# Performance work log

Measured on AMD Instinct MI355X. Metric: run time of the kernel, lower is better.

The kernel has to match this reference:

```python
import jax, jax.numpy as jnp
import numpy as np

N_NODES = 100000
N_EDGES = 1600000
N_FEAT = 128
HIDDEN = 128
N_CLASSES = 10
N_GRAPHS = 512


def setup_inputs() -> dict:
    key = jax.random.key(0)
    ks = jax.random.split(key, 20)

    def lin(k, fan_in, fan_out, bias=True):
        kw, kb = jax.random.split(k)
        s = 1.0 / np.sqrt(fan_in)
        W = jax.random.uniform(kw, (fan_in, fan_out), jnp.float32, -s, s)
        if bias:
            b = jax.random.uniform(kb, (fan_out,), jnp.float32, -s, s)
            return W, b
        return W

    x = jax.random.normal(ks[0], (N_NODES, N_FEAT), jnp.float32)
    edge_index = jax.random.randint(ks[1], (2, N_EDGES), 0, N_NODES)
    batch = jnp.sort(jax.random.randint(ks[2], (N_NODES,), 0, N_GRAPHS))

    w1l, b1 = lin(ks[3], N_FEAT, HIDDEN)
    w1r = lin(ks[4], N_FEAT, HIDDEN, bias=False)
    w2l, b2 = lin(ks[5], HIDDEN, HIDDEN)
    w2r = lin(ks[6], HIDDEN, HIDDEN, bias=False)
    w3l, b3 = lin(ks[7], HIDDEN, HIDDEN)
    w3r = lin(ks[8], HIDDEN, HIDDEN, bias=False)
    gate_w, gate_b = lin(ks[9], HIDDEN, 1)
    lin1_w, lin1_b = lin(ks[10], HIDDEN, HIDDEN)
    lin2_w, lin2_b = lin(ks[11], HIDDEN, N_CLASSES)

    return dict(x=x, edge_index=edge_index, batch=batch,
                w1l=w1l, b1=b1, w1r=w1r,
                w2l=w2l, b2=b2, w2r=w2r,
                w3l=w3l, b3=b3, w3r=w3r,
                gate_w=gate_w, gate_b=gate_b,
                lin1_w=lin1_w, lin1_b=lin1_b,
                lin2_w=lin2_w, lin2_b=lin2_b)


def _sage_conv(x, src, dst, Wl, bl, Wr, n_nodes):
    # PyG SAGEConv(mean): out = lin_l(mean_{j in N(i)} x_j) + lin_r(x_i)
    msg_sum = jax.ops.segment_sum(x[src], dst, num_segments=n_nodes)
    cnt = jax.ops.segment_sum(jnp.ones((src.shape[0], 1), x.dtype), dst,
                              num_segments=n_nodes)
    mean = msg_sum / jnp.maximum(cnt, 1.0)
    return mean @ Wl + bl + x @ Wr


def reference(x, edge_index, batch,
              w1l, b1, w1r, w2l, b2, w2r, w3l, b3, w3r,
              gate_w, gate_b, lin1_w, lin1_b, lin2_w, lin2_b):
    n = x.shape[0]
    src, dst = edge_index[0], edge_index[1]

    h = jax.nn.relu(_sage_conv(x, src, dst, w1l, b1, w1r, n))
    h = jax.nn.relu(_sage_conv(h, src, dst, w2l, b2, w2r, n))
    h = jax.nn.relu(_sage_conv(h, src, dst, w3l, b3, w3r, n))

    # AttentionalAggregation: scatter-softmax of gate over graph segments
    gate = h @ gate_w + gate_b                                  # [N, 1]
    m = jax.ops.segment_max(gate, batch, num_segments=N_GRAPHS)  # [G, 1]
    e = jnp.exp(gate - m[batch])
    s = jax.ops.segment_sum(e, batch, num_segments=N_GRAPHS)     # [G, 1]
    alpha = e / s[batch]
    pooled = jax.ops.segment_sum(alpha * h, batch, num_segments=N_GRAPHS)  # [G, H]

    out = jax.nn.relu(pooled @ lin1_w + lin1_b)
    # dropout is identity in eval mode
    out = out @ lin2_w + lin2_b
    return jax.nn.log_softmax(out, axis=-1)
```

## Files before the change

### kernel.cpp

```cpp
#include <hip/hip_runtime.h>
#include <stdint.h>

#define N_NODES 100000
#define N_EDGES 1600000
#define NF 128
#define NG 512
#define NC 10

#define NBUCK ((N_NODES + 255) / 256)
#define EPB 4096

#define KSTRIDE 136
#define GEMM_B ((N_NODES + 127) / 128)

#define CVT_B 6250
#define BT_B 384
#define BOUNDS_B 3
#define COUNT_B ((N_EDGES + EPB - 1) / EPB)

typedef short short8 __attribute__((ext_vector_type(8)));
typedef float f32x4 __attribute__((ext_vector_type(4)));

__device__ __forceinline__ unsigned short f2b(float f) {
    unsigned u = __float_as_uint(f);
    u += 0x7fffu + ((u >> 16) & 1u);
    return (unsigned short)(u >> 16);
}
__device__ __forceinline__ unsigned cvt2(float lo, float hi) {
    unsigned r;
    asm("v_cvt_pk_bf16_f32 %0, %1, %2" : "=v"(r) : "v"(lo), "v"(hi));
    return r;
}
__device__ __forceinline__ float lo16(unsigned v) { return __uint_as_float(v << 16); }
__device__ __forceinline__ float hi16(unsigned v) { return __uint_as_float(v & 0xffff0000u); }

__global__ __launch_bounds__(256) void prep_kernel(const float* __restrict__ x, unsigned short* __restrict__ xb,
                                                   const float* __restrict__ w1l, const float* __restrict__ w1r,
                                                   const float* __restrict__ w2l, const float* __restrict__ w2r,
                                                   const float* __restrict__ w3l, const float* __restrict__ w3r,
                                                   unsigned short* __restrict__ Bt,
                                                   const int* __restrict__ batch, int* __restrict__ gstart,
                                                   const int* __restrict__ dst, int* __restrict__ bcount) {
    const int b = blockIdx.x, t = threadIdx.x;
    if (b < CVT_B) {
        int i = b * 256 + t;
        const float4* ip = (const float4*)x;
        float4 a = ip[2 * i], c = ip[2 * i + 1];
        uint4 o;
        o.x = cvt2(a.x, a.y);
        o.y = cvt2(a.z, a.w);
        o.z = cvt2(c.x, c.y);
        o.w = cvt2(c.z, c.w);
        ((uint4*)xb)[i] = o;
    } else if (b < CVT_B + BT_B) {
        int i = (b - CVT_B) * 256 + t;
        int layer = i / (128 * 256);
        int r = i % (128 * 256);
        int n = r / 256, k = r % 256;
        const float* wl = (layer == 0) ? w1l : (layer == 1) ? w2l : w3l;
        const float* wr = (layer == 0) ? w1r : (layer == 1) ? w2r : w3r;
        float v = (k < 128) ? wl[k * 128 + n] : wr[(k - 128) * 128 + n];
        Bt[i] = f2b(v);
    } else if (b < CVT_B + BT_B + BOUNDS_B) {
        int g = (b - CVT_B - BT_B) * 256 + t;
        if (g > NG) return;
        int lo = 0, hi = N_NODES;
        while (lo < hi) {
            int mid = (lo + hi) >> 1;
            if (batch[mid] < g) lo = mid + 1; else hi = mid;
        }
        gstart[g] = lo;
    } else {
        __shared__ int h[NBUCK];
        for (int i = t; i < NBUCK; i += 256) h[i] = 0;
        __syncthreads();
        const int base = (b - CVT_B - BT_B - BOUNDS_B) * EPB;
        const int lim = min(base + EPB, N_EDGES);
        for (int i = base + t; i < lim; i += 256) atomicAdd(&h[dst[i] >> 8], 1);
        __syncthreads();
        for (int i = t; i < NBUCK; i += 256)
            if (h[i]) atomicAdd(&bcount[i], h[i]);
    }
}

__global__ __launch_bounds__(512) void bucket_scan(const int* __restrict__ bcount, int* __restrict__ bbase,
                                                   int* __restrict__ gcursor, int* __restrict__ rowptr) {
    __shared__ int sh[512];
    const int t = threadIdx.x;
    int v = (t < NBUCK) ? bcount[t] : 0;
    sh[t] = v;
    __syncthreads();
    for (int off = 1; off < 512; off <<= 1) {
        int u = (t >= off) ? sh[t - off] : 0;
        __syncthreads();
        sh[t] += u;
        __syncthreads();
    }
    if (t < NBUCK) {
        int e = sh[t] - v;
        bbase[t] = e;
        gcursor[t] = e;
    }
    if (t == NBUCK - 1) bbase[NBUCK] = sh[t];
    if (t == 0) rowptr[N_NODES] = N_EDGES;
}

__global__ __launch_bounds__(256) void bucket_scatter(const int* __restrict__ src, const int* __restrict__ dst,
                                                      int* __restrict__ gcursor, unsigned* __restrict__ brec) {
    __shared__ int h[NBUCK];
    for (int i = threadIdx.x; i < NBUCK; i += 256) h[i] = 0;
    __syncthreads();
    const int base = blockIdx.x * EPB;
    const int lim = min(base + EPB, N_EDGES);
    for (int i = base + threadIdx.x; i < lim; i += 256) atomicAdd(&h[dst[i] >> 8], 1);
    __syncthreads();
    for (int i = threadIdx.x; i < NBUCK; i += 256) {
        int c = h[i];
        if (c) h[i] = atomicAdd(&gcursor[i], c);
    }
    __syncthreads();
    for (int i = base + threadIdx.x; i < lim; i += 256) {
        int d = dst[i];
        int pos = atomicAdd(&h[d >> 8], 1);
        brec[pos] = ((unsigned)(d & 255) << 17) | (unsigned)src[i];
    }
}

__global__ __launch_bounds__(256) void bucket_fill(const unsigned* __restrict__ brec, const int* __restrict__ bbase,
                                                   int* __restrict__ rowptr, int* __restrict__ eidx) {
    __shared__ int nh[256];
    __shared__ int sc[256];
    const int b = blockIdx.x, t = threadIdx.x;
    const int beg = bbase[b], end = bbase[b + 1];
    nh[t] = 0;
    __syncthreads();
    for (int i = beg + t; i < end; i += 256) atomicAdd(&nh[brec[i] >> 17], 1);
    __syncthreads();
    int cnt = nh[t];
    sc[t] = cnt;
    __syncthreads();
    for (int off = 1; off < 256; off <<= 1) {
        int u = (t >= off) ? sc[t - off] : 0;
        __syncthreads();
        sc[t] += u;
        __syncthreads();
    }
    int excl = sc[t] - cnt;
    int node = b * 256 + t;
    if (node < N_NODES) rowptr[node] = beg + excl;
    nh[t] = beg + excl;
    __syncthreads();
    for (int i = beg + t; i < end; i += 256) {
        unsigned r = brec[i];
        int pos = atomicAdd(&nh[r >> 17], 1);
        eidx[pos] = (int)(r & 0x1FFFFu);
    }
}

__global__ __launch_bounds__(256) void agg_kernel(const unsigned short* __restrict__ F,
                                                  const int* __restrict__ rowptr,
                                                  const int* __restrict__ eidx,
                                                  unsigned short* __restrict__ M) {
    int node = blockIdx.x * 4 + (threadIdx.x >> 6);
    if (node >= N_NODES) return;
    const int lane = threadIdx.x & 63;
    const int quad = lane >> 4, ql = lane & 15;
    const int beg = rowptr[node], end = rowptr[node + 1];
    const char* Fb = (const char*)F;
    const unsigned qoff = (unsigned)ql << 4;

    float a0 = 0.f, a1 = 0.f, a2 = 0.f, a3 = 0.f, a4 = 0.f, a5 = 0.f, a6 = 0.f, a7 = 0.f;

    for (int cs = beg; cs < end; cs += 64) {
        int e = cs + lane;
        int idx = eidx[e < end ? e : end - 1];
        int n = end - cs;
        if (n > 64) n = 64;
        const int nfull = n >> 4;
        int l = quad;
        for (int g = 0; g < nfull; ++g, l += 16) {
            int r0 = __shfl(idx, l);
            int r1 = __shfl(idx, l + 4);
            int r2 = __shfl(idx, l + 8);
            int r3 = __shfl(idx, l + 12);
            uint4 v0 = *(const uint4*)(Fb + (((unsigned)r0 << 8) | qoff));
            uint4 v1 = *(const uint4*)(Fb + (((unsigned)r1 << 8) | qoff));
            uint4 v2 = *(const uint4*)(Fb + (((unsigned)r2 << 8) | qoff));
            uint4 v3 = *(const uint4*)(Fb + (((unsigned)r3 << 8) | qoff));
            a0 += lo16(v0.x) + lo16(v1.x) + lo16(v2.x) + lo16(v3.x);
            a1 += hi16(v0.x) + hi16(v1.x) + hi16(v2.x) + hi16(v3.x);
            a2 += lo16(v0.y) + lo16(v1.y) + lo16(v2.y) + lo16(v3.y);
            a3 += hi16(v0.y) + hi16(v1.y) + hi16(v2.y) + hi16(v3.y);
            a4 += lo16(v0.z) + lo16(v1.z) + lo16(v2.z) + lo16(v3.z);
            a5 += hi16(v0.z) + hi16(v1.z) + hi16(v2.z) + hi16(v3.z);
            a6 += lo16(v0.w) + lo16(v1.w) + lo16(v2.w) + lo16(v3.w);
            a7 += hi16(v0.w) + hi16(v1.w) + hi16(v2.w) + hi16(v3.w);
        }
        const int base = nfull << 4;
        for (int it = base; it < n; it += 4) {
            int l0 = it + quad;
            int r0 = __shfl(idx, l0 < n ? l0 : n - 1);
            float s0 = (l0 < n) ? 1.f : 0.f;
            uint4 v0 = *(const uint4*)(Fb + (((unsigned)r0 << 8) | qoff));
            a0 += s0 * lo16(v0.x); a1 += s0 * hi16(v0.x);
            a2 += s0 * lo16(v0.y); a3 += s0 * hi16(v0.y);
            a4 += s0 * lo16(v0.z); a5 += s0 * hi16(v0.z);
            a6 += s0 * lo16(v0.w); a7 += s0 * hi16(v0.w);
        }
    }

    a0 += __shfl_xor(a0, 16); a0 += __shfl_xor(a0, 32);
    a1 += __shfl_xor(a1, 16); a1 += __shfl_xor(a1, 32);
    a2 += __shfl_xor(a2, 16); a2 += __shfl_xor(a2, 32);
    a3 += __shfl_xor(a3, 16); a3 += __shfl_xor(a3, 32);
    a4 += __shfl_xor(a4, 16); a4 += __shfl_xor(a4, 32);
    a5 += __shfl_xor(a5, 16); a5 += __shfl_xor(a5, 32);
    a6 += __shfl_xor(a6, 16); a6 += __shfl_xor(a6, 32);
    a7 += __shfl_xor(a7, 16); a7 += __shfl_xor(a7, 32);

    if (quad == 0) {
        float inv = 1.0f / (float)max(end - beg, 1);
        uint4 o;
        o.x = cvt2(a0 * inv, a1 * inv);
        o.y = cvt2(a2 * inv, a3 * inv);
        o.z = cvt2(a4 * inv, a5 * inv);
        o.w = cvt2(a6 * inv, a7 * inv);
        ((uint4*)M)[(size_t)node * 16 + ql] = o;
    }
}

__global__ __launch_bounds__(256, 4) void gemm_kernel(const unsigned short* __restrict__ Am,
                                                      const unsigned short* __restrict__ Ax,
                                                      const unsigned short* __restrict__ Bt,
                                                      const float* __restrict__ bias,
                                                      unsigned short* __restrict__ Out,
                                                      const float* __restrict__ gatew,
                                                      const float* __restrict__ gateb,
                                                      float* __restrict__ gate) {
    const int t = threadIdx.x;
    const int wave = t >> 6, lane = t & 63;
    const int lrow = lane & 15, quad = lane >> 4;
    const int row0 = blockIdx.x * 128 + wave * 32;

    __shared__ __attribute__((aligned(16))) unsigned short Bs[128 * KSTRIDE];

    f32x4 acc[2][8];
#pragma unroll
    for (int i = 0; i < 2; ++i)
#pragma unroll
        for (int j = 0; j < 8; ++j) acc[i][j] = (f32x4){0.f, 0.f, 0.f, 0.f};

    int arow0 = row0 + lrow;          if (arow0 > N_NODES - 1) arow0 = N_NODES - 1;
    int arow1 = row0 + 16 + lrow;     if (arow1 > N_NODES - 1) arow1 = N_NODES - 1;

    for (int p = 0; p < 2; ++p) {
        if (p) __syncthreads();
#pragma unroll
        for (int i = 0; i < 8; ++i) {
            int u = t + i * 256;
            int r = u >> 4, seg = u & 15;
            *(uint4*)(Bs + r * KSTRIDE + seg * 8) =
                *(const uint4*)(Bt + (size_t)r * 256 + p * 128 + seg * 8);
        }
        __syncthreads();

        const unsigned short* Aarr = p ? Ax : Am;
#pragma unroll
        for (int c = 0; c < 4; ++c) {
            const int kb = c * 32 + quad * 8;
            short8 af0 = *(const short8*)(Aarr + (size_t)arow0 * 128 + kb);
            short8 af1 = *(const short8*)(Aarr + (size_t)arow1 * 128 + kb);
#pragma unroll
            for (int nt = 0; nt < 8; ++nt) {
                short8 bf = *(const short8*)(Bs + (nt * 16 + lrow) * KSTRIDE + kb);
                acc[0][nt] = __builtin_amdgcn_mfma_f32_16x16x32_bf16(af0, bf, acc[0][nt], 0, 0, 0);
                acc[1][nt] = __builtin_amdgcn_mfma_f32_16x16x32_bf16(af1, bf, acc[1][nt], 0, 0, 0);
            }
        }
    }

    float gpart[2][4];
#pragma unroll
    for (int i = 0; i < 2; ++i)
#pragma unroll
        for (int r = 0; r < 4; ++r) gpart[i][r] = 0.f;

#pragma unroll
    for (int nt = 0; nt < 8; ++nt) {
        int col = nt * 16 + lrow;
        float bc = bias[col];
        float gw = gatew ? gatew[col] : 0.f;
#pragma unroll
        for (int i = 0; i < 2; ++i) {
            int rbase = row0 + i * 16 + quad * 4;
#pragma unroll
            for (int r = 0; r < 4; ++r) {
                int row = rbase + r;
                float v = fmaxf(acc[i][nt][r] + bc, 0.f);
                if (row < N_NODES) gpart[i][r] += v * gw;
                unsigned sv = (unsigned)f2b(v);
                unsigned nb = (unsigned)__shfl_xor((int)sv, 1);
                if (((lrow & 1) == 0) && row < N_NODES)
                    *(unsigned*)(Out + (size_t)row * 128 + col) = sv | (nb << 16);
            }
        }
    }
    if (gatew) {
        float gb = gateb[0];
#pragma unroll
        for (int i = 0; i < 2; ++i) {
#pragma unroll
            for (int r = 0; r < 4; ++r) {
                float g = gpart[i][r];
                g += __shfl_xor(g, 1);
                g += __shfl_xor(g, 2);
                g += __shfl_xor(g, 4);
                g += __shfl_xor(g, 8);
                if (lrow == 0) {
                    int row = row0 + i * 16 + quad * 4 + r;
                    if (row < N_NODES) gate[row] = g + gb;
                }
            }
        }
    }
}

__global__ __launch_bounds__(64) void pool_mlp_kernel(const unsigned short* __restrict__ h,
                                                      const float* __restrict__ gate,
                                                      const int* __restrict__ gstart,
                                                      const float* __restrict__ l1w,
                                                      const float* __restrict__ l1b,
                                                      const float* __restrict__ l2w,
                                                      const float* __restrict__ l2b,
                                                      float* __restrict__ out) {
    int g = blockIdx.x;
    int lane = threadIdx.x;
    __shared__ float pooled_s[128];
    __shared__ float hid_s[128];

    int beg = gstart[g], end = gstart[g + 1];

    float m = -INFINITY;
    for (int i = beg + lane; i < end; i += 64) m = fmaxf(m, gate[i]);
#pragma unroll
    for (int o = 32; o; o >>= 1) m = fmaxf(m, __shfl_xor(m, o));
    float s = 0.f;
    for (int i = beg + lane; i < end; i += 64) s += expf(gate[i] - m);
#pragma unroll
    for (int o = 32; o; o >>= 1) s += __shfl_xor(s, o);
    float invs = (s > 0.f) ? 1.0f / s : 0.f;

    float ax = 0.f, ay = 0.f;
    const unsigned* hb = (const unsigned*)h;
    int i = beg;
    for (; i + 2 <= end; i += 2) {
        float w0 = expf(gate[i] - m) * invs;
        float w1 = expf(gate[i + 1] - m) * invs;
        unsigned v0 = hb[(size_t)i * 64 + lane];
        unsigned v1 = hb[(size_t)(i + 1) * 64 + lane];
        ax += w0 * lo16(v0) + w1 * lo16(v1);
        ay += w0 * hi16(v0) + w1 * hi16(v1);
    }
    for (; i < end; ++i) {
        float w = expf(gate[i] - m) * invs;
        unsigned v = hb[(size_t)i * 64 + lane];
        ax += w * lo16(v);
        ay += w * hi16(v);
    }
    pooled_s[2 * lane] = ax;
    pooled_s[2 * lane + 1] = ay;
    __syncthreads();

    float h0 = l1b[lane], h1 = l1b[lane + 64];
    for (int k = 0; k < 128; ++k) {
        float pv = pooled_s[k];
        h0 += pv * l1w[k * 128 + lane];
        h1 += pv * l1w[k * 128 + lane + 64];
    }
    hid_s[lane] = fmaxf(h0, 0.f);
    hid_s[lane + 64] = fmaxf(h1, 0.f);
    __syncthreads();

    float o10 = 0.f;
    if (lane < NC) {
        o10 = l2b[lane];
        for (int k = 0; k < 128; ++k) o10 += hid_s[k] * l2w[k * NC + lane];
    }
    float mm = -INFINITY;
#pragma unroll
    for (int j = 0; j < NC; ++j) mm = fmaxf(mm, __shfl(o10, j));
    float ss = 0.f;
#pragma unroll
    for (int j = 0; j < NC; ++j) ss += expf(__shfl(o10, j) - mm);
    float lse = mm + logf(ss);
    if (lane < NC) out[g * NC + lane] = o10 - lse;
}

extern "C" void kernel_launch(void* const* d_in, const int* in_sizes, int n_in,
                              void* d_out, int out_size, void* d_ws, size_t ws_size,
                              hipStream_t stream) {
    const float* x   = (const float*)d_in[0];
    const int* ei    = (const int*)d_in[1];
    const int* batch = (const int*)d_in[2];
    const float* w1l = (const float*)d_in[3];
    const float* b1  = (const float*)d_in[4];
    const float* w1r = (const float*)d_in[5];
    const float* w2l = (const float*)d_in[6];
    const float* b2  = (const float*)d_in[7];
    const float* w2r = (const float*)d_in[8];
    const float* w3l = (const float*)d_in[9];
    const float* b3  = (const float*)d_in[10];
    const float* w3r = (const float*)d_in[11];
    const float* gw  = (const float*)d_in[12];
    const float* gb  = (const float*)d_in[13];
    const float* l1w = (const float*)d_in[14];
    const float* l1b = (const float*)d_in[15];
    const float* l2w = (const float*)d_in[16];
    const float* l2b = (const float*)d_in[17];
    float* out = (float*)d_out;

    const int* src = ei;
    const int* dst = ei + N_EDGES;

    char* base = (char*)d_ws;
    size_t off = 0;
    auto carve = [&](size_t bytes) -> void* {
        void* r = base + off;
        off = (off + bytes + 255) & ~(size_t)255;
        return r;
    };
    int* rowptr         = (int*)carve((size_t)(N_NODES + 1) * 4);
    int* eidx           = (int*)carve((size_t)N_EDGES * 4);
    unsigned short* Bt  = (unsigned short*)carve((size_t)3 * 128 * 256 * 2);
    unsigned short* xb  = (unsigned short*)carve((size_t)N_NODES * NF * 2);
    unsigned short* mn  = (unsigned short*)carve((size_t)N_NODES * NF * 2);
    unsigned short* hA  = (unsigned short*)carve((size_t)N_NODES * NF * 2);
    unsigned short* hB  = (unsigned short*)carve((size_t)N_NODES * NF * 2);
    float* gate         = (float*)carve((size_t)N_NODES * 4);
    int* gstart         = (int*)carve(513 * 4);
    int* bcount         = (int*)carve((NBUCK + 1) * 4);
    int* bbase          = (int*)carve((NBUCK + 1) * 4);
    int* gcursor        = (int*)carve((NBUCK + 1) * 4);
    unsigned* brec      = (unsigned*)mn;

    hipMemsetAsync(bcount, 0, (size_t)NBUCK * 4, stream);

    prep_kernel<<<CVT_B + BT_B + BOUNDS_B + COUNT_B, 256, 0, stream>>>(
        x, xb, w1l, w1r, w2l, w2r, w3l, w3r, Bt, batch, gstart, dst, bcount);

    bucket_scan<<<1, 512, 0, stream>>>(bcount, bbase, gcursor, rowptr);
    bucket_scatter<<<COUNT_B, 256, 0, stream>>>(src, dst, gcursor, brec);
    bucket_fill<<<NBUCK, 256, 0, stream>>>(brec, bbase, rowptr, eidx);

    const int AGG_B = (N_NODES + 3) / 4;

    agg_kernel<<<AGG_B, 256, 0, stream>>>(xb, rowptr, eidx, mn);
    gemm_kernel<<<GEMM_B, 256, 0, stream>>>(mn, xb, Bt, b1, hA, nullptr, nullptr, nullptr);
    agg_kernel<<<AGG_B, 256, 0, stream>>>(hA, rowptr, eidx, mn);
    gemm_kernel<<<GEMM_B, 256, 0, stream>>>(mn, hA, Bt + 32768, b2, hB, nullptr, nullptr, nullptr);
    agg_kernel<<<AGG_B, 256, 0, stream>>>(hB, rowptr, eidx, mn);
    gemm_kernel<<<GEMM_B, 256, 0, stream>>>(mn, hB, Bt + 65536, b3, hA, gw, gb, gate);

    pool_mlp_kernel<<<NG, 64, 0, stream>>>(hA, gate, gstart, l1w, l1b, l2w, l2b, out);
}
```

Measured before the change: 457.9 us.

## Fuse neighbor mean aggregation and SAGE GEMM into one per-layer kernel

Each SAGE layer now runs as a single kernel. Each 1024-thread block aggregates 16 nodes, one wave per node, into an LDS tile, then eight waves run 16x16 MFMA tiles over the concatenated [mean | self] features. This drops the global round trip of the mean matrix and three launches per forward pass. The gate projection is now built from per-column-tile partial sums added atomically into a zeroed buffer, and the gate bias is dropped because it cancels in the softmax. In exchange, weights are read from global or L2 per wave instead of staged in LDS, half the waves sit idle during the GEMM phase, and extra atomics are added.

```diff
diff --git a/kernel.cpp b/kernel.cpp
--- a/kernel.cpp
+++ b/kernel.cpp
@@ -10,8 +10,8 @@
 #define NBUCK ((N_NODES + 255) / 256)
 #define EPB 4096
 
-#define KSTRIDE 136
-#define GEMM_B ((N_NODES + 127) / 128)
+#define ASTR 136
+#define FUSED_B (N_NODES / 16)
 
 #define CVT_B 6250
 #define BT_B 384
@@ -157,14 +157,20 @@
     }
 }
 
-__global__ __launch_bounds__(256) void agg_kernel(const unsigned short* __restrict__ F,
-                                                  const int* __restrict__ rowptr,
-                                                  const int* __restrict__ eidx,
-                                                  unsigned short* __restrict__ M) {
-    int node = blockIdx.x * 4 + (threadIdx.x >> 6);
-    if (node >= N_NODES) return;
-    const int lane = threadIdx.x & 63;
+__global__ __launch_bounds__(1024, 8) void fused_kernel(const unsigned short* __restrict__ F,
+                                                        const int* __restrict__ rowptr,
+                                                        const int* __restrict__ eidx,
+                                                        const unsigned short* __restrict__ Bt,
+                                                        const float* __restrict__ bias,
+                                                        unsigned short* __restrict__ Out,
+                                                        const float* __restrict__ gatew,
+                                                        float* __restrict__ gate) {
+    __shared__ __attribute__((aligned(16))) unsigned short A_lds[16 * ASTR];
+    const int t = threadIdx.x;
+    const int w = t >> 6, lane = t & 63;
     const int quad = lane >> 4, ql = lane & 15;
+    const int row0 = blockIdx.x * 16;
+    const int node = row0 + w;
     const int beg = rowptr[node], end = rowptr[node + 1];
     const char* Fb = (const char*)F;
     const unsigned qoff = (unsigned)ql << 4;
@@ -225,102 +231,52 @@
         o.y = cvt2(a2 * inv, a3 * inv);
         o.z = cvt2(a4 * inv, a5 * inv);
         o.w = cvt2(a6 * inv, a7 * inv);
-        ((uint4*)M)[(size_t)node * 16 + ql] = o;
-    }
-}
-
-__global__ __launch_bounds__(256, 4) void gemm_kernel(const unsigned short* __restrict__ Am,
-                                                      const unsigned short* __restrict__ Ax,
-                                                      const unsigned short* __restrict__ Bt,
-                                                      const float* __restrict__ bias,
-                                                      unsigned short* __restrict__ Out,
-                                                      const float* __restrict__ gatew,
-                                                      const float* __restrict__ gateb,
-                                                      float* __restrict__ gate) {
-    const int t = threadIdx.x;
-    const int wave = t >> 6, lane = t & 63;
-    const int lrow = lane & 15, quad = lane >> 4;
-    const int row0 = blockIdx.x * 128 + wave * 32;
-
-    __shared__ __attribute__((aligned(16))) unsigned short Bs[128 * KSTRIDE];
-
-    f32x4 acc[2][8];
-#pragma unroll
-    for (int i = 0; i < 2; ++i)
-#pragma unroll
-        for (int j = 0; j < 8; ++j) acc[i][j] = (f32x4){0.f, 0.f, 0.f, 0.f};
-
-    int arow0 = row0 + lrow;          if (arow0 > N_NODES - 1) arow0 = N_NODES - 1;
-    int arow1 = row0 + 16 + lrow;     if (arow1 > N_NODES - 1) arow1 = N_NODES - 1;
-
-    for (int p = 0; p < 2; ++p) {
-        if (p) __syncthreads();
-#pragma unroll
-        for (int i = 0; i < 8; ++i) {
-            int u = t + i * 256;
-            int r = u >> 4, seg = u & 15;
-            *(uint4*)(Bs + r * KSTRIDE + seg * 8) =
-                *(const uint4*)(Bt + (size_t)r * 256 + p * 128 + seg * 8);
-        }
-        __syncthreads();
-
-        const unsigned short* Aarr = p ? Ax : Am;
-#pragma unroll
-        for (int c = 0; c < 4; ++c) {
-            const int kb = c * 32 + quad * 8;
-            short8 af0 = *(const short8*)(Aarr + (size_t)arow0 * 128 + kb);
-            short8 af1 = *(const short8*)(Aarr + (size_t)arow1 * 128 + kb);
-#pragma unroll
-            for (int nt = 0; nt < 8; ++nt) {
-                short8 bf = *(const short8*)(Bs + (nt * 16 + lrow) * KSTRIDE + kb);
-                acc[0][nt] = __builtin_amdgcn_mfma_f32_16x16x32_bf16(af0, bf, acc[0][nt], 0, 0, 0);
-                acc[1][nt] = __builtin_amdgcn_mfma_f32_16x16x32_bf16(af1, bf, acc[1][nt], 0, 0, 0);
-            }
-        }
-    }
-
-    float gpart[2][4];
-#pragma unroll
-    for (int i = 0; i < 2; ++i)
-#pragma unroll
-        for (int r = 0; r < 4; ++r) gpart[i][r] = 0.f;
-
-#pragma unroll
-    for (int nt = 0; nt < 8; ++nt) {
-        int col = nt * 16 + lrow;
-        float bc = bias[col];
-        float gw = gatew ? gatew[col] : 0.f;
-#pragma unroll
-        for (int i = 0; i < 2; ++i) {
-            int rbase = row0 + i * 16 + quad * 4;
-#pragma unroll
-            for (int r = 0; r < 4; ++r) {
-                int row = rbase + r;
-                float v = fmaxf(acc[i][nt][r] + bc, 0.f);
-                if (row < N_NODES) gpart[i][r] += v * gw;
-                unsigned sv = (unsigned)f2b(v);
-                unsigned nb = (unsigned)__shfl_xor((int)sv, 1);
-                if (((lrow & 1) == 0) && row < N_NODES)
-                    *(unsigned*)(Out + (size_t)row * 128 + col) = sv | (nb << 16);
-            }
-        }
+        *(uint4*)(A_lds + w * ASTR + ql * 8) = o;
+    }
+    __syncthreads();
+    if (w >= 8) return;
+
+    const int lrow = ql;
+    f32x4 acc = (f32x4){0.f, 0.f, 0.f, 0.f};
+    const unsigned short* Brow = Bt + ((size_t)(w * 16 + lrow)) * 256;
+    const unsigned short* Arow = F + (size_t)(row0 + lrow) * 128;
+#pragma unroll
+    for (int c = 0; c < 4; ++c) {
+        const int kb = c * 32 + quad * 8;
+        short8 af = *(const short8*)(A_lds + lrow * ASTR + kb);
+        short8 bf = *(const short8*)(Brow + kb);
+        acc = __builtin_amdgcn_mfma_f32_16x16x32_bf16(af, bf, acc, 0, 0, 0);
+    }
+#pragma unroll
+    for (int c = 0; c < 4; ++c) {
+        const int kb = c * 32 + quad * 8;
+        short8 af = *(const short8*)(Arow + kb);
+        short8 bf = *(const short8*)(Brow + 128 + kb);
+        acc = __builtin_amdgcn_mfma_f32_16x16x32_bf16(af, bf, acc, 0, 0, 0);
+    }
+
+    const int col = w * 16 + lrow;
+    const float bc = bias[col];
+    const float gw = gatew ? gatew[col] : 0.f;
+    float gsum[4];
+#pragma unroll
+    for (int r = 0; r < 4; ++r) {
+        float v = fmaxf(acc[r] + bc, 0.f);
+        gsum[r] = v * gw;
+        unsigned sv = (unsigned)f2b(v);
+        unsigned nb = (unsigned)__shfl_xor((int)sv, 1);
+        if ((lrow & 1) == 0)
+            *(unsigned*)(Out + (size_t)(row0 + quad * 4 + r) * 128 + col) = sv | (nb << 16);
     }
     if (gatew) {
-        float gb = gateb[0];
-#pragma unroll
-        for (int i = 0; i < 2; ++i) {
-#pragma unroll
-            for (int r = 0; r < 4; ++r) {
-                float g = gpart[i][r];
-                g += __shfl_xor(g, 1);
-                g += __shfl_xor(g, 2);
-                g += __shfl_xor(g, 4);
-                g += __shfl_xor(g, 8);
-                if (lrow == 0) {
-                    int row = row0 + i * 16 + quad * 4 + r;
-                    if (row < N_NODES) gate[row] = g + gb;
-                }
-            }
+#pragma unroll
+        for (int r = 0; r < 4; ++r) {
+            float g = gsum[r];
+            g += __shfl_xor(g, 1);
+            g += __shfl_xor(g, 2);
+            g += __shfl_xor(g, 4);
+            g += __shfl_xor(g, 8);
+            if (lrow == 0) atomicAdd(&gate[row0 + quad * 4 + r], g);
         }
     }
 }
@@ -418,6 +374,7 @@
     const float* l2w = (const float*)d_in[16];
     const float* l2b = (const float*)d_in[17];
     float* out = (float*)d_out;
+    (void)gb;
 
     const int* src = ei;
     const int* dst = ei + N_EDGES;
@@ -433,17 +390,17 @@
     int* eidx           = (int*)carve((size_t)N_EDGES * 4);
     unsigned short* Bt  = (unsigned short*)carve((size_t)3 * 128 * 256 * 2);
     unsigned short* xb  = (unsigned short*)carve((size_t)N_NODES * NF * 2);
-    unsigned short* mn  = (unsigned short*)carve((size_t)N_NODES * NF * 2);
     unsigned short* hA  = (unsigned short*)carve((size_t)N_NODES * NF * 2);
     unsigned short* hB  = (unsigned short*)carve((size_t)N_NODES * NF * 2);
+    unsigned* brec      = (unsigned*)carve((size_t)N_EDGES * 4);
     float* gate         = (float*)carve((size_t)N_NODES * 4);
     int* gstart         = (int*)carve(513 * 4);
     int* bcount         = (int*)carve((NBUCK + 1) * 4);
     int* bbase          = (int*)carve((NBUCK + 1) * 4);
     int* gcursor        = (int*)carve((NBUCK + 1) * 4);
-    unsigned* brec      = (unsigned*)mn;
 
     hipMemsetAsync(bcount, 0, (size_t)NBUCK * 4, stream);
+    hipMemsetAsync(gate, 0, (size_t)N_NODES * 4, stream);
 
     prep_kernel<<<CVT_B + BT_B + BOUNDS_B + COUNT_B, 256, 0, stream>>>(
         x, xb, w1l, w1r, w2l, w2r, w3l, w3r, Bt, batch, gstart, dst, bcount);
@@ -452,14 +409,9 @@
     bucket_scatter<<<COUNT_B, 256, 0, stream>>>(src, dst, gcursor, brec);
     bucket_fill<<<NBUCK, 256, 0, stream>>>(brec, bbase, rowptr, eidx);
 
-    const int AGG_B = (N_NODES + 3) / 4;
-
-    agg_kernel<<<AGG_B, 256, 0, stream>>>(xb, rowptr, eidx, mn);
-    gemm_kernel<<<GEMM_B, 256, 0, stream>>>(mn, xb, Bt, b1, hA, nullptr, nullptr, nullptr);
-    agg_kernel<<<AGG_B, 256, 0, stream>>>(hA, rowptr, eidx, mn);
-    gemm_kernel<<<GEMM_B, 256, 0, stream>>>(mn, hA, Bt + 32768, b2, hB, nullptr, nullptr, nullptr);
-    agg_kernel<<<AGG_B, 256, 0, stream>>>(hB, rowptr, eidx, mn);
-    gemm_kernel<<<GEMM_B, 256, 0, stream>>>(mn, hB, Bt + 65536, b3, hA, gw, gb, gate);
+    fused_kernel<<<FUSED_B, 1024, 0, stream>>>(xb, rowptr, eidx, Bt, b1, hA, nullptr, nullptr);
+    fused_kernel<<<FUSED_B, 1024, 0, stream>>>(hA, rowptr, eidx, Bt + 32768, b2, hB, nullptr, nullptr);
+    fused_kernel<<<FUSED_B, 1024, 0, stream>>>(hB, rowptr, eidx, Bt + 65536, b3, hA, gw, gate);
 
     pool_mlp_kernel<<<NG, 64, 0, stream>>>(hA, gate, gstart, l1w, l1b, l2w, l2b, out);
 }
```

After: 595.9 us. +30.1%, slower.
